# Kernel optimization log

Hardware: AMD Instinct MI355X
Metric: run time of the kernel (lower is better)

## Reference

```python
import math
import jax, jax.numpy as jnp
import numpy as np

B = 256          # graphs per batch
N0 = 512         # nodes per graph
DEG = 16         # avg degree
E = B * N0 * DEG # total edges
F_IN = 160
H = 64
RATIO = 0.11
NUM_CLASSES = 2


def setup_inputs() -> dict:
    key = jax.random.key(0)
    ks = jax.random.split(key, 20)
    x = jax.random.normal(ks[0], (B * N0, F_IN), jnp.float32)
    # within-graph random edges: src/dst local in [0, N0) plus graph offset
    eg = E // B
    off = (jnp.arange(B, dtype=jnp.int32) * N0)[:, None]
    src = (jax.random.randint(ks[1], (B, eg), 0, N0, jnp.int32) + off).reshape(-1)
    dst = (jax.random.randint(ks[2], (B, eg), 0, N0, jnp.int32) + off).reshape(-1)
    edge_index = jnp.stack([src, dst], 0)
    s = lambda fan: 1.0 / np.sqrt(fan)
    inp = {
        'x': x,
        'edge_index': edge_index,
        'conv1_Wr': jax.random.normal(ks[3], (F_IN, H), jnp.float32) * s(F_IN),
        'conv1_Wl': jax.random.normal(ks[4], (F_IN, H), jnp.float32) * s(F_IN),
        'conv1_b': jnp.zeros((H,), jnp.float32),
        'convs_Wr': jax.random.normal(ks[5], (5, H, H), jnp.float32) * s(H),
        'convs_Wl': jax.random.normal(ks[6], (5, H, H), jnp.float32) * s(H),
        'convs_b': jnp.zeros((5, H), jnp.float32),
        'pools_Wr': jax.random.normal(ks[7], (2, H, 1), jnp.float32) * s(H),
        'pools_Wl': jax.random.normal(ks[8], (2, H, 1), jnp.float32) * s(H),
        'pools_b': jnp.zeros((2, 1), jnp.float32),
        'lin1_W': jax.random.normal(ks[9], (6 * H, H), jnp.float32) * s(6 * H),
        'lin1_b': jnp.zeros((H,), jnp.float32),
        'lin2_W': jax.random.normal(ks[10], (H, NUM_CLASSES), jnp.float32) * s(H),
        'lin2_b': jnp.zeros((NUM_CLASSES,), jnp.float32),
    }
    return inp


def _gconv(x, src, dst, emask, Wr, Wl, b, n_nodes):
    # PyG GraphConv(aggr='mean'): lin_rel(mean_{j->i} x_j) + lin_root(x)
    msg = x[src] * emask[:, None]                              # [E, F]
    agg = jax.ops.segment_sum(msg, dst, num_segments=n_nodes)  # [N, F]
    deg = jax.ops.segment_sum(emask, dst, num_segments=n_nodes)
    agg = agg / jnp.maximum(deg, 1.0)[:, None]
    return agg @ Wr + b + x @ Wl


def _sag_pool(x, src, dst, emask, Wr, Wl, b, n_per, k):
    n_nodes = B * n_per
    score = _gconv(x, src, dst, emask, Wr, Wl, b, n_nodes)[:, 0]   # [N]
    _, idx = jax.lax.top_k(score.reshape(B, n_per), k)             # [B, k]
    perm = (idx + (jnp.arange(B, dtype=jnp.int32) * n_per)[:, None]).reshape(-1)
    new_x = x[perm] * jnp.tanh(score[perm])[:, None]
    newpos = jnp.full((n_nodes,), -1, jnp.int32).at[perm].set(
        jnp.arange(B * k, dtype=jnp.int32))
    ns, nd = newpos[src], newpos[dst]
    valid = (ns >= 0) & (nd >= 0)
    new_emask = emask * valid.astype(emask.dtype)
    return new_x, jnp.where(valid, ns, 0), jnp.where(valid, nd, 0), new_emask


def _gmp(x, n_per):  # global_mean_pool with equal-size graphs
    return x.reshape(B, n_per, -1).mean(axis=1)


def reference(x, edge_index, conv1_Wr, conv1_Wl, conv1_b, convs_Wr, convs_Wl,
              convs_b, pools_Wr, pools_Wl, pools_b, lin1_W, lin1_b,
              lin2_W, lin2_b):
    src, dst = edge_index[0], edge_index[1]
    emask = jnp.ones(src.shape, x.dtype)
    n = N0
    x = jax.nn.relu(_gconv(x, src, dst, emask, conv1_Wr, conv1_Wl, conv1_b, B * n))
    xs = [_gmp(x, n)]
    for i in range(5):
        x = jax.nn.relu(_gconv(x, src, dst, emask, convs_Wr[i], convs_Wl[i],
                               convs_b[i], B * n))
        xs.append(_gmp(x, n))
        if i % 2 == 0 and i < 4:
            j = i // 2
            k = math.ceil(RATIO * n)
            x, src, dst, emask = _sag_pool(x, src, dst, emask, pools_Wr[j],
                                           pools_Wl[j], pools_b[j], n, k)
            n = k
    h = jnp.concatenate(xs, axis=-1)          # JumpingKnowledge('cat') -> [B, 6H]
    h = jax.nn.relu(h @ lin1_W + lin1_b)
    h = h @ lin2_W + lin2_b                   # dropout is identity in eval mode
    return jax.nn.log_softmax(h, axis=-1)
```

## Files before the change

### kernel.cpp

```cpp
#include <hip/hip_runtime.h>
#include <math.h>

namespace {
constexpr int NB   = 256;
constexpr int EPG  = 8192;
constexpr int ETOT = NB * EPG;
}

__global__ __launch_bounds__(1024)
void mono(const float* __restrict__ x,
          const int* __restrict__ esrc, const int* __restrict__ edst,
          const float* __restrict__ c1Wr, const float* __restrict__ c1Wl,
          const float* __restrict__ c1b,
          const float* __restrict__ cWr, const float* __restrict__ cWl,
          const float* __restrict__ cb,
          const float* __restrict__ pwr, const float* __restrict__ pwl,
          const float* __restrict__ pb,
          const float* __restrict__ l1W, const float* __restrict__ l1b,
          const float* __restrict__ l2W, const float* __restrict__ l2b,
          float* __restrict__ out)
{
  __shared__ float zlds[512 * 64];
  __shared__ unsigned short csrbuf[EPG];
  __shared__ __align__(16) unsigned long long u2[512];
  __shared__ float wpf[2048];
  __shared__ float xsl[384];
  __shared__ int scnt;
  unsigned int* hist  = reinterpret_cast<unsigned int*>(u2);
  unsigned int* start = hist + 512;
  const int g = blockIdx.x, t = threadIdx.x;
  const int gbase = g * 512, ebase = g * EPG;
  const int lane = t & 63, w = t >> 6;
  const int ndbase = w * 32;

  auto stage_chunk = [&](int c, int p) {
    const int xb  = p ? 8192  : 0;
    const int wrO = p ? 18432 : 16384;
    const int wlO = p ? 22528 : 20480;
    #pragma unroll
    for (int i = 0; i < 2; ++i) {
      const int slot = t + i * 1024;
      const int r = slot >> 2, q = slot & 3;
      const float* gp = &x[(size_t)(gbase + r) * 160 + c * 16 + q * 4];
      float* lp = zlds + xb + (size_t)(i * 1024 + w * 64) * 4;
      __builtin_amdgcn_global_load_lds(
          (const __attribute__((address_space(1))) unsigned int*)gp,
          (__attribute__((address_space(3))) unsigned int*)lp, 16, 0, 0);
    }
    {
      const float* gp = &c1Wr[c * 1024 + t];
      float* lp = zlds + wrO + (size_t)(w * 64);
      __builtin_amdgcn_global_load_lds(
          (const __attribute__((address_space(1))) unsigned int*)gp,
          (__attribute__((address_space(3))) unsigned int*)lp, 4, 0, 0);
    }
    {
      const float* gp = &c1Wl[c * 1024 + t];
      float* lp = zlds + wlO + (size_t)(w * 64);
      __builtin_amdgcn_global_load_lds(
          (const __attribute__((address_space(1))) unsigned int*)gp,
          (__attribute__((address_space(3))) unsigned int*)lp, 4, 0, 0);
    }
  };

  if (t < 512) hist[t] = 0;
  if (t == 0) scnt = 0;
  __syncthreads();
  stage_chunk(0, 0);
  for (int e = t; e < EPG; e += 1024)
    atomicAdd(&hist[edst[ebase + e] - gbase], 1u);
  __syncthreads();
  {
    unsigned int* sA = reinterpret_cast<unsigned int*>(wpf);
    unsigned int* sB = sA + 512;
    if (t < 512) sA[t] = hist[t];
    __syncthreads();
    unsigned int *pa = sA, *pb = sB;
    for (int off = 1; off < 512; off <<= 1) {
      if (t < 512) {
        unsigned int v = pa[t];
        if (t >= off) v += pa[t - off];
        pb[t] = v;
      }
      __syncthreads();
      unsigned int* tmp = pa; pa = pb; pb = tmp;
    }
    if (t < 512) start[t] = pa[t] - hist[t];
    __syncthreads();
    unsigned int* cur = pb;
    if (t < 512) cur[t] = start[t];
    __syncthreads();
    for (int e = t; e < EPG; e += 1024) {
      const int sl = esrc[ebase + e] - gbase;
      const int dl = edst[ebase + e] - gbase;
      const unsigned int pos = atomicAdd(&cur[dl], 1u);
      csrbuf[pos] = (unsigned short)sl;
    }
  }
  __syncthreads();
  float zacc[32], xla[32];
  #pragma unroll
  for (int i = 0; i < 32; ++i) { zacc[i] = 0.f; xla[i] = 0.f; }
  #pragma unroll 1
  for (int c = 0; c < 10; ++c) {
    if (c < 9) stage_chunk(c + 1, (c + 1) & 1);
    const int p   = c & 1;
    const int xb  = p ? 8192  : 0;
    const int wrO = p ? 18432 : 16384;
    const int wlO = p ? 22528 : 20480;
    #pragma unroll 1
    for (int k4 = 0; k4 < 4; ++k4) {
      const int kb = k4 * 4;
      const float wr0 = zlds[wrO + (kb+0)*64 + lane], wr1 = zlds[wrO + (kb+1)*64 + lane],
                  wr2 = zlds[wrO + (kb+2)*64 + lane], wr3 = zlds[wrO + (kb+3)*64 + lane];
      const float wl0 = zlds[wlO + (kb+0)*64 + lane], wl1 = zlds[wlO + (kb+1)*64 + lane],
                  wl2 = zlds[wlO + (kb+2)*64 + lane], wl3 = zlds[wlO + (kb+3)*64 + lane];
      #pragma unroll
      for (int i = 0; i < 32; ++i) {
        const float4 xv = *reinterpret_cast<const float4*>(
            &zlds[xb + (ndbase + i) * 16 + kb]);
        float za = zacc[i], xa = xla[i];
        za = fmaf(xv.x, wr0, za); za = fmaf(xv.y, wr1, za);
        za = fmaf(xv.z, wr2, za); za = fmaf(xv.w, wr3, za);
        xa = fmaf(xv.x, wl0, xa); xa = fmaf(xv.y, wl1, xa);
        xa = fmaf(xv.z, wl2, xa); xa = fmaf(xv.w, wl3, xa);
        zacc[i] = za; xla[i] = xa;
      }
    }
    __syncthreads();
  }
  #pragma unroll
  for (int i = 0; i < 32; ++i)
    zlds[(ndbase + i) * 64 + lane] = zacc[i];
  __syncthreads();
  {
    const float bv = c1b[lane];
    float psum = 0.f;
    #pragma unroll 1
    for (int i = 0; i < 32; ++i) {
      const int nd = ndbase + i;
      const unsigned int s = start[nd], d = hist[nd];
      float a0 = 0.f, a1 = 0.f, a2 = 0.f, a3 = 0.f;
      unsigned int j = 0;
      for (; j + 4 <= d; j += 4) {
        const int i0 = csrbuf[s+j], i1 = csrbuf[s+j+1],
                  i2 = csrbuf[s+j+2], i3 = csrbuf[s+j+3];
        a0 += zlds[i0*64 + lane]; a1 += zlds[i1*64 + lane];
        a2 += zlds[i2*64 + lane]; a3 += zlds[i3*64 + lane];
      }
      for (; j < d; ++j) a0 += zlds[csrbuf[s+j]*64 + lane];
      float v = ((a0 + a1) + (a2 + a3)) / (float)(d > 0 ? d : 1) + xla[i] + bv;
      v = fmaxf(v, 0.f);
      zacc[i] = v;
      psum += v;
    }
    __syncthreads();
    #pragma unroll
    for (int i = 0; i < 32; ++i)
      zlds[(ndbase + i) * 64 + lane] = zacc[i];
    wpf[w * 64 + lane] = psum;
    __syncthreads();
    if (t < 64) {
      float s = 0.f;
      #pragma unroll
      for (int ww = 0; ww < 16; ++ww) s += wpf[ww*64 + t];
      xsl[0 + t] = s * (1.f/512.f);
    }
  }
  #pragma unroll
  for (int i = 0; i < 32; ++i) { zacc[i] = 0.f; xla[i] = 0.f; }
  {
    float* w_r = wpf;
    float* w_l = wpf + 1024;
    #pragma unroll 1
    for (int c = 0; c < 4; ++c) {
      __syncthreads();
      w_r[t] = cWr[c * 1024 + t];
      w_l[t] = cWl[c * 1024 + t];
      __syncthreads();
      #pragma unroll 1
      for (int k4 = 0; k4 < 4; ++k4) {
        const int kb = k4 * 4;
        const float wr0 = w_r[(kb+0)*64 + lane], wr1 = w_r[(kb+1)*64 + lane],
                    wr2 = w_r[(kb+2)*64 + lane], wr3 = w_r[(kb+3)*64 + lane];
        const float wl0 = w_l[(kb+0)*64 + lane], wl1 = w_l[(kb+1)*64 + lane],
                    wl2 = w_l[(kb+2)*64 + lane], wl3 = w_l[(kb+3)*64 + lane];
        #pragma unroll
        for (int i = 0; i < 32; ++i) {
          const float4 xv = *reinterpret_cast<const float4*>(
              &zlds[(ndbase + i) * 64 + c * 16 + kb]);
          float za = zacc[i], xa = xla[i];
          za = fmaf(xv.x, wr0, za); za = fmaf(xv.y, wr1, za);
          za = fmaf(xv.z, wr2, za); za = fmaf(xv.w, wr3, za);
          xa = fmaf(xv.x, wl0, xa); xa = fmaf(xv.y, wl1, xa);
          xa = fmaf(xv.z, wl2, xa); xa = fmaf(xv.w, wl3, xa);
          zacc[i] = za; xla[i] = xa;
        }
      }
    }
  }
  __syncthreads();
  #pragma unroll
  for (int i = 0; i < 32; ++i)
    zlds[(ndbase + i) * 64 + lane] = zacc[i];
  __syncthreads();
  {
    const float bv = cb[lane];
    float psum = 0.f;
    #pragma unroll 1
    for (int i = 0; i < 32; ++i) {
      const int nd = ndbase + i;
      const unsigned int s = start[nd], d = hist[nd];
      float a0 = 0.f, a1 = 0.f, a2 = 0.f, a3 = 0.f;
      unsigned int j = 0;
      for (; j + 4 <= d; j += 4) {
        const int i0 = csrbuf[s+j], i1 = csrbuf[s+j+1],
                  i2 = csrbuf[s+j+2], i3 = csrbuf[s+j+3];
        a0 += zlds[i0*64 + lane]; a1 += zlds[i1*64 + lane];
        a2 += zlds[i2*64 + lane]; a3 += zlds[i3*64 + lane];
      }
      for (; j < d; ++j) a0 += zlds[csrbuf[s+j]*64 + lane];
      float v = ((a0 + a1) + (a2 + a3)) / (float)(d > 0 ? d : 1) + xla[i] + bv;
      v = fmaxf(v, 0.f);
      zacc[i] = v;
      psum += v;
    }
    __syncthreads();
    #pragma unroll
    for (int i = 0; i < 32; ++i)
      zlds[(ndbase + i) * 64 + lane] = zacc[i];
    wpf[w * 64 + lane] = psum;
    __syncthreads();
    if (t < 64) {
      float s = 0.f;
      #pragma unroll
      for (int ww = 0; ww < 16; ++ww) s += wpf[ww*64 + t];
      xsl[64 + t] = s * (1.f/512.f);
    }
    __syncthreads();
  }
  {
    float* zs     = wpf;
    float* swl    = wpf + 512;
    float* sscore = wpf + 1024;
    const float pwrv = pwr[lane], pwlv = pwl[lane];
    for (int nd = w; nd < 512; nd += 16) {
      const float v = zlds[nd*64 + lane];
      float a = v * pwrv, b = v * pwlv;
      #pragma unroll
      for (int off = 32; off > 0; off >>= 1) {
        a += __shfl_xor(a, off);
        b += __shfl_xor(b, off);
      }
      if (lane == 0) { zs[nd] = a; swl[nd] = b; }
    }
    __syncthreads();
    if (t < 512) {
      const unsigned int s = start[t], d = hist[t];
      float a = 0.f;
      for (unsigned int j = 0; j < d; ++j) a += zs[csrbuf[s + j]];
      sscore[t] = a / fmaxf((float)d, 1.f) + pb[0] + swl[t];
    }
    __syncthreads();
    unsigned long long* keys = u2;
    if (t < 512) {
      unsigned int u = __float_as_uint(sscore[t]);
      u = (u & 0x80000000u) ? ~u : (u | 0x80000000u);
      keys[t] = ((unsigned long long)u << 32) | (unsigned int)(~(unsigned int)t);
    }
    __syncthreads();
    for (int kk = 2; kk <= 512; kk <<= 1) {
      for (int j = kk >> 1; j > 0; j >>= 1) {
        if (t < 512) {
          const int ixj = t ^ j;
          if (ixj > t) {
            const unsigned long long a = keys[t], bk = keys[ixj];
            const bool up = ((t & kk) == 0);
            if (up ? (a < bk) : (a > bk)) { keys[t] = bk; keys[ixj] = a; }
          }
        }
        __syncthreads();
      }
    }
    short* np = reinterpret_cast<short*>(csrbuf);
    if (t < 512) np[t] = -1;
    __syncthreads();
    if (t < 57)
      np[(int)(~(unsigned int)(keys[t] & 0xffffffffull))] = (short)t;
    __syncthreads();
    float xr[4];
    int nr = 0;
    for (int r = w * 4; r < w * 4 + 4 && r < 57; ++r) {
      const int old = (int)(~(unsigned int)(keys[r] & 0xffffffffull));
      xr[nr++] = zlds[old*64 + lane] * tanhf(sscore[old]);
    }
    if (t < 64) wpf[t] = 0.f;
    if (t == 0) scnt = 0;
    __syncthreads();
    nr = 0;
    for (int r = w * 4; r < w * 4 + 4 && r < 57; ++r)
      zlds[r*64 + lane] = xr[nr++];
    unsigned int* eb = reinterpret_cast<unsigned int*>(zlds + 16384);
    for (int e = t; e < EPG; e += 1024) {
      const int sl = esrc[ebase + e] - gbase;
      const int dl = edst[ebase + e] - gbase;
      const int ns = np[sl], nd2 = np[dl];
      if (ns >= 0 && nd2 >= 0) {
        const int slot = atomicAdd(&scnt, 1);
        eb[slot] = (unsigned int)ns | ((unsigned int)nd2 << 16);
        atomicAdd(&wpf[nd2], 1.f);
      }
    }
    __syncthreads();
  }
  const int m0 = scnt;
  float* X   = zlds;
  float* Z   = zlds + 4096;
  float* ACC = zlds + 8192;
  float* deg = wpf;
  float* w_s = wpf + 512;
  unsigned int* eb  = reinterpret_cast<unsigned int*>(zlds + 16384);
  unsigned int* eb1 = reinterpret_cast<unsigned int*>(zlds + 24576);

  auto conv57 = [&](int n, const unsigned int* edges, int m,
                    const float* Wr, const float* Wl, const float* bias,
                    int xs_off) {
    for (int i = t; i < n*64; i += 1024) { Z[i] = 0.f; ACC[i] = 0.f; }
    __syncthreads();
    for (int kc = 0; kc < 4; ++kc) {
      w_s[t] = Wr[kc*1024 + t];
      __syncthreads();
      for (int r = w; r < n; r += 16) {
        float za = 0.f;
        #pragma unroll
        for (int k = 0; k < 16; ++k)
          za = fmaf(X[r*64 + kc*16 + k], w_s[k*64 + lane], za);
        Z[r*64 + lane] += za;
      }
      __syncthreads();
    }
    for (int e = w; e < m; e += 16) {
      const unsigned int pr = edges[e];
      const int sl = pr & 0xffff, dl = pr >> 16;
      atomicAdd(&ACC[dl*64 + lane], Z[sl*64 + lane]);
    }
    __syncthreads();
    for (int i = t; i < n*64; i += 1024) {
      const int r = i >> 6, f = i & 63;
      Z[i] = ACC[i] / fmaxf(deg[r], 1.f) + bias[f];
    }
    __syncthreads();
    for (int kc = 0; kc < 4; ++kc) {
      w_s[t] = Wl[kc*1024 + t];
      __syncthreads();
      for (int r = w; r < n; r += 16) {
        float za = 0.f;
        #pragma unroll
        for (int k = 0; k < 16; ++k)
          za = fmaf(X[r*64 + kc*16 + k], w_s[k*64 + lane], za);
        Z[r*64 + lane] += za;
      }
      __syncthreads();
    }
    for (int i = t; i < n*64; i += 1024) X[i] = fmaxf(Z[i], 0.f);
    __syncthreads();
    float psum = 0.f;
    for (int r = w; r < n; r += 16) psum += X[r*64 + lane];
    Z[w*64 + lane] = psum;
    __syncthreads();
    if (t < 64) {
      float s = 0.f;
      #pragma unroll
      for (int ww = 0; ww < 16; ++ww) s += Z[ww*64 + t];
      xsl[xs_off + t] = s / (float)n;
    }
    __syncthreads();
  };

  conv57(57, eb, m0, cWr + 4096, cWl + 4096, cb + 64, 128);
  conv57(57, eb, m0, cWr + 8192, cWl + 8192, cb + 128, 192);

  {
    float* zs1 = wpf + 1536;
    float* sw1 = wpf + 1600;
    float* ss1 = wpf + 1664;
    const float pwrv = pwr[64 + lane], pwlv = pwl[64 + lane];
    for (int r = w; r < 57; r += 16) {
      float a = X[r*64 + lane] * pwrv, b = X[r*64 + lane] * pwlv;
      #pragma unroll
      for (int off = 32; off > 0; off >>= 1) {
        a += __shfl_xor(a, off);
        b += __shfl_xor(b, off);
      }
      if (lane == 0) { zs1[r] = a; sw1[r] = b; }
    }
    if (t >= 64 && t < 128) ACC[t - 64] = 0.f;
    __syncthreads();
    for (int e = t; e < m0; e += 1024) {
      const unsigned int pr = eb[e];
      atomicAdd(&ACC[pr >> 16], zs1[pr & 0xffff]);
    }
    __syncthreads();
    if (t < 57) ss1[t] = ACC[t] / fmaxf(deg[t], 1.f) + pb[1] + sw1[t];
    __syncthreads();
    unsigned long long* keys = u2;
    if (t < 64) {
      unsigned long long key = 0ull;
      if (t < 57) {
        unsigned int u = __float_as_uint(ss1[t]);
        u = (u & 0x80000000u) ? ~u : (u | 0x80000000u);
        key = ((unsigned long long)u << 32) | (unsigned int)(~(unsigned int)t);
      }
      keys[t] = key;
    }
    __syncthreads();
    for (int kk = 2; kk <= 64; kk <<= 1) {
      for (int j = kk >> 1; j > 0; j >>= 1) {
        if (t < 64) {
          const int ixj = t ^ j;
          if (ixj > t) {
            const unsigned long long a = keys[t], bk = keys[ixj];
            const bool up = ((t & kk) == 0);
            if (up ? (a < bk) : (a > bk)) { keys[t] = bk; keys[ixj] = a; }
          }
        }
        __syncthreads();
      }
    }
    short* np1 = reinterpret_cast<short*>(csrbuf);
    if (t < 64) np1[t] = -1;
    __syncthreads();
    if (t < 7)
      np1[(int)(~(unsigned int)(keys[t] & 0xffffffffull))] = (short)t;
    __syncthreads();
    float xv7 = 0.f;
    int old7 = -1;
    if (w < 7 && w * 4 == w * 4) {
      old7 = (int)(~(unsigned int)(keys[w] & 0xffffffffull));
      xv7 = X[old7*64 + lane] * tanhf(ss1[old7]);
    }
    if (t < 64) deg[t] = 0.f;
    if (t == 0) scnt = 0;
    __syncthreads();
    if (w < 7) X[w*64 + lane] = xv7;
    for (int e = t; e < m0; e += 1024) {
      const unsigned int pr = eb[e];
      const int ns = np1[pr & 0xffff], nd2 = np1[pr >> 16];
      if (ns >= 0 && nd2 >= 0) {
        const int slot = atomicAdd(&scnt, 1);
        eb1[slot] = (unsigned int)ns | ((unsigned int)nd2 << 16);
        atomicAdd(&deg[nd2], 1.f);
      }
    }
    __syncthreads();
  }
  const int m1 = scnt;

  conv57(7, eb1, m1, cWr + 12288, cWl + 12288, cb + 192, 256);
  conv57(7, eb1, m1, cWr + 16384, cWl + 16384, cb + 256, 320);

  if (t < 64) {
    float acc = l1b[t];
    for (int j = 0; j < 384; ++j) acc = fmaf(xsl[j], l1W[j*64 + t], acc);
    wpf[t] = fmaxf(acc, 0.f);
  }
  __syncthreads();
  if (t < 2) {
    float a2 = l2b[t];
    for (int f2 = 0; f2 < 64; ++f2) a2 = fmaf(wpf[f2], l2W[f2*2 + t], a2);
    wpf[64 + t] = a2;
  }
  __syncthreads();
  if (t < 2) {
    const float mx = fmaxf(wpf[64], wpf[65]);
    const float lse = mx + logf(expf(wpf[64]-mx) + expf(wpf[65]-mx));
    out[g*2 + t] = wpf[64 + t] - lse;
  }
}

extern "C" void kernel_launch(void* const* d_in, const int* in_sizes, int n_in,
                              void* d_out, int out_size, void* d_ws, size_t ws_size,
                              hipStream_t stream)
{
  (void)in_sizes; (void)n_in; (void)d_ws; (void)ws_size; (void)out_size;
  const float* x    = (const float*)d_in[0];
  const int*   ei   = (const int*)d_in[1];
  const float* c1Wr = (const float*)d_in[2];
  const float* c1Wl = (const float*)d_in[3];
  const float* c1b  = (const float*)d_in[4];
  const float* cWr  = (const float*)d_in[5];
  const float* cWl  = (const float*)d_in[6];
  const float* cb   = (const float*)d_in[7];
  const float* pWr  = (const float*)d_in[8];
  const float* pWl  = (const float*)d_in[9];
  const float* pb   = (const float*)d_in[10];
  const float* l1W  = (const float*)d_in[11];
  const float* l1b  = (const float*)d_in[12];
  const float* l2W  = (const float*)d_in[13];
  const float* l2b  = (const float*)d_in[14];
  float* out = (float*)d_out;
  const int* esrc = ei;
  const int* edst = ei + ETOT;

  mono<<<NB, 1024, 0, stream>>>(x, esrc, edst, c1Wr, c1Wl, c1b,
                                cWr, cWl, cb, pWr, pWl, pb,
                                l1W, l1b, l2W, l2b, out);
}
```

Before: 320.4 us.

## Use wavefront shuffles for scan and bitonic sorts, fuse conv57 matmuls

Replaces the LDS Hillis-Steele prefix scan with a wave-level shuffle scan plus a cross-wave offset, cutting the number of block barriers. The 512-key bitonic sort keeps keys in registers and uses shuffles for distances below 64, touching LDS only for larger strides. The 64-key sort runs entirely inside one wavefront. conv57 stages the full 64x64 weights in LDS once per matmul instead of in four chunks and fuses ReLU and the pooling sum into the second matmul, which removes several barriers and passes over the data.

```diff
diff --git a/kernel.cpp b/kernel.cpp
--- a/kernel.cpp
+++ b/kernel.cpp
@@ -28,6 +28,7 @@
   __shared__ int scnt;
   unsigned int* hist  = reinterpret_cast<unsigned int*>(u2);
   unsigned int* start = hist + 512;
+  unsigned int* curp  = reinterpret_cast<unsigned int*>(wpf);
   const int g = blockIdx.x, t = threadIdx.x;
   const int gbase = g * 512, ebase = g * EPG;
   const int lane = t & 63, w = t >> 6;
@@ -71,29 +72,31 @@
     atomicAdd(&hist[edst[ebase + e] - gbase], 1u);
   __syncthreads();
   {
-    unsigned int* sA = reinterpret_cast<unsigned int*>(wpf);
-    unsigned int* sB = sA + 512;
-    if (t < 512) sA[t] = hist[t];
-    __syncthreads();
-    unsigned int *pa = sA, *pb = sB;
-    for (int off = 1; off < 512; off <<= 1) {
-      if (t < 512) {
-        unsigned int v = pa[t];
-        if (t >= off) v += pa[t - off];
-        pb[t] = v;
-      }
-      __syncthreads();
-      unsigned int* tmp = pa; pa = pb; pb = tmp;
-    }
-    if (t < 512) start[t] = pa[t] - hist[t];
-    __syncthreads();
-    unsigned int* cur = pb;
-    if (t < 512) cur[t] = start[t];
+    unsigned int v = 0;
+    if (t < 512) {
+      v = hist[t];
+      #pragma unroll
+      for (int off = 1; off < 64; off <<= 1) {
+        const unsigned int up = __shfl_up(v, off);
+        if (lane >= off) v += up;
+      }
+      if (lane == 63)
+        reinterpret_cast<unsigned int*>(wpf)[1024 + w] = v;
+    }
+    __syncthreads();
+    if (t < 512) {
+      unsigned int off = 0;
+      for (int i = 0; i < w; ++i)
+        off += reinterpret_cast<unsigned int*>(wpf)[1024 + i];
+      const unsigned int st = off + v - hist[t];
+      start[t] = st;
+      curp[t]  = st;
+    }
     __syncthreads();
     for (int e = t; e < EPG; e += 1024) {
       const int sl = esrc[ebase + e] - gbase;
       const int dl = edst[ebase + e] - gbase;
-      const unsigned int pos = atomicAdd(&cur[dl], 1u);
+      const unsigned int pos = atomicAdd(&curp[dl], 1u);
       csrbuf[pos] = (unsigned short)sl;
     }
   }
@@ -262,26 +265,36 @@
       sscore[t] = a / fmaxf((float)d, 1.f) + pb[0] + swl[t];
     }
     __syncthreads();
-    unsigned long long* keys = u2;
+    unsigned long long k = 0ull;
     if (t < 512) {
       unsigned int u = __float_as_uint(sscore[t]);
       u = (u & 0x80000000u) ? ~u : (u | 0x80000000u);
-      keys[t] = ((unsigned long long)u << 32) | (unsigned int)(~(unsigned int)t);
-    }
-    __syncthreads();
+      k = ((unsigned long long)u << 32) | (unsigned int)(~(unsigned int)t);
+    }
     for (int kk = 2; kk <= 512; kk <<= 1) {
       for (int j = kk >> 1; j > 0; j >>= 1) {
-        if (t < 512) {
-          const int ixj = t ^ j;
-          if (ixj > t) {
-            const unsigned long long a = keys[t], bk = keys[ixj];
-            const bool up = ((t & kk) == 0);
-            if (up ? (a < bk) : (a > bk)) { keys[t] = bk; keys[ixj] = a; }
+        if (j >= 64) {
+          if (t < 512) u2[t] = k;
+          __syncthreads();
+          unsigned long long kp = 0ull;
+          if (t < 512) kp = u2[t ^ j];
+          __syncthreads();
+          if (t < 512) {
+            const bool keep_max = (((t & kk) == 0) == ((t & j) == 0));
+            k = keep_max ? (k >= kp ? k : kp) : (k >= kp ? kp : k);
           }
+        } else if (t < 512) {
+          const unsigned int lo = __shfl_xor((unsigned int)k, j);
+          const unsigned int hi = __shfl_xor((unsigned int)(k >> 32), j);
+          const unsigned long long kp = ((unsigned long long)hi << 32) | lo;
+          const bool keep_max = (((t & kk) == 0) == ((t & j) == 0));
+          k = keep_max ? (k >= kp ? k : kp) : (k >= kp ? kp : k);
         }
-        __syncthreads();
-      }
-    }
+      }
+    }
+    if (t < 512) u2[t] = k;
+    __syncthreads();
+    unsigned long long* keys = u2;
     short* np = reinterpret_cast<short*>(csrbuf);
     if (t < 512) np[t] = -1;
     __syncthreads();
@@ -318,60 +331,51 @@
   float* Z   = zlds + 4096;
   float* ACC = zlds + 8192;
   float* deg = wpf;
-  float* w_s = wpf + 512;
   unsigned int* eb  = reinterpret_cast<unsigned int*>(zlds + 16384);
   unsigned int* eb1 = reinterpret_cast<unsigned int*>(zlds + 24576);
 
   auto conv57 = [&](int n, const unsigned int* edges, int m,
                     const float* Wr, const float* Wl, const float* bias,
                     int xs_off) {
-    for (int i = t; i < n*64; i += 1024) { Z[i] = 0.f; ACC[i] = 0.f; }
-    __syncthreads();
-    for (int kc = 0; kc < 4; ++kc) {
-      w_s[t] = Wr[kc*1024 + t];
-      __syncthreads();
-      for (int r = w; r < n; r += 16) {
-        float za = 0.f;
-        #pragma unroll
-        for (int k = 0; k < 16; ++k)
-          za = fmaf(X[r*64 + kc*16 + k], w_s[k*64 + lane], za);
-        Z[r*64 + lane] += za;
-      }
-      __syncthreads();
-    }
+    float* Wfull = zlds + 12288;
+    for (int i = t; i < n*64; i += 1024) ACC[i] = 0.f;
+    #pragma unroll
+    for (int i = 0; i < 4; ++i) Wfull[t + i*1024] = Wr[t + i*1024];
+    __syncthreads();
+    for (int r = w; r < n; r += 16) {
+      float za = 0.f;
+      for (int k = 0; k < 64; ++k)
+        za = fmaf(X[r*64 + k], Wfull[k*64 + lane], za);
+      Z[r*64 + lane] = za;
+    }
+    __syncthreads();
     for (int e = w; e < m; e += 16) {
       const unsigned int pr = edges[e];
-      const int sl = pr & 0xffff, dl = pr >> 16;
-      atomicAdd(&ACC[dl*64 + lane], Z[sl*64 + lane]);
-    }
+      atomicAdd(&ACC[(pr >> 16)*64 + lane], Z[(pr & 0xffff)*64 + lane]);
+    }
+    #pragma unroll
+    for (int i = 0; i < 4; ++i) Wfull[t + i*1024] = Wl[t + i*1024];
     __syncthreads();
     for (int i = t; i < n*64; i += 1024) {
       const int r = i >> 6, f = i & 63;
       Z[i] = ACC[i] / fmaxf(deg[r], 1.f) + bias[f];
     }
     __syncthreads();
-    for (int kc = 0; kc < 4; ++kc) {
-      w_s[t] = Wl[kc*1024 + t];
-      __syncthreads();
-      for (int r = w; r < n; r += 16) {
-        float za = 0.f;
-        #pragma unroll
-        for (int k = 0; k < 16; ++k)
-          za = fmaf(X[r*64 + kc*16 + k], w_s[k*64 + lane], za);
-        Z[r*64 + lane] += za;
-      }
-      __syncthreads();
-    }
-    for (int i = t; i < n*64; i += 1024) X[i] = fmaxf(Z[i], 0.f);
-    __syncthreads();
     float psum = 0.f;
-    for (int r = w; r < n; r += 16) psum += X[r*64 + lane];
-    Z[w*64 + lane] = psum;
+    for (int r = w; r < n; r += 16) {
+      float za = Z[r*64 + lane];
+      for (int k = 0; k < 64; ++k)
+        za = fmaf(X[r*64 + k], Wfull[k*64 + lane], za);
+      za = fmaxf(za, 0.f);
+      X[r*64 + lane] = za;
+      psum += za;
+    }
+    ACC[w*64 + lane] = psum;
     __syncthreads();
     if (t < 64) {
       float s = 0.f;
       #pragma unroll
-      for (int ww = 0; ww < 16; ++ww) s += Z[ww*64 + t];
+      for (int ww = 0; ww < 16; ++ww) s += ACC[ww*64 + t];
       xsl[xs_off + t] = s / (float)n;
     }
     __syncthreads();
@@ -403,30 +407,26 @@
     __syncthreads();
     if (t < 57) ss1[t] = ACC[t] / fmaxf(deg[t], 1.f) + pb[1] + sw1[t];
     __syncthreads();
+    if (w == 0) {
+      unsigned long long k1 = 0ull;
+      if (lane < 57) {
+        unsigned int u = __float_as_uint(ss1[lane]);
+        u = (u & 0x80000000u) ? ~u : (u | 0x80000000u);
+        k1 = ((unsigned long long)u << 32) | (unsigned int)(~(unsigned int)lane);
+      }
+      for (int kk = 2; kk <= 64; kk <<= 1) {
+        for (int j = kk >> 1; j > 0; j >>= 1) {
+          const unsigned int lo = __shfl_xor((unsigned int)k1, j);
+          const unsigned int hi = __shfl_xor((unsigned int)(k1 >> 32), j);
+          const unsigned long long kp = ((unsigned long long)hi << 32) | lo;
+          const bool keep_max = (((lane & kk) == 0) == ((lane & j) == 0));
+          k1 = keep_max ? (k1 >= kp ? k1 : kp) : (k1 >= kp ? kp : k1);
+        }
+      }
+      u2[lane] = k1;
+    }
+    __syncthreads();
     unsigned long long* keys = u2;
-    if (t < 64) {
-      unsigned long long key = 0ull;
-      if (t < 57) {
-        unsigned int u = __float_as_uint(ss1[t]);
-        u = (u & 0x80000000u) ? ~u : (u | 0x80000000u);
-        key = ((unsigned long long)u << 32) | (unsigned int)(~(unsigned int)t);
-      }
-      keys[t] = key;
-    }
-    __syncthreads();
-    for (int kk = 2; kk <= 64; kk <<= 1) {
-      for (int j = kk >> 1; j > 0; j >>= 1) {
-        if (t < 64) {
-          const int ixj = t ^ j;
-          if (ixj > t) {
-            const unsigned long long a = keys[t], bk = keys[ixj];
-            const bool up = ((t & kk) == 0);
-            if (up ? (a < bk) : (a > bk)) { keys[t] = bk; keys[ixj] = a; }
-          }
-        }
-        __syncthreads();
-      }
-    }
     short* np1 = reinterpret_cast<short*>(csrbuf);
     if (t < 64) np1[t] = -1;
     __syncthreads();
@@ -434,9 +434,8 @@
       np1[(int)(~(unsigned int)(keys[t] & 0xffffffffull))] = (short)t;
     __syncthreads();
     float xv7 = 0.f;
-    int old7 = -1;
-    if (w < 7 && w * 4 == w * 4) {
-      old7 = (int)(~(unsigned int)(keys[w] & 0xffffffffull));
+    if (w < 7) {
+      const int old7 = (int)(~(unsigned int)(keys[w] & 0xffffffffull));
       xv7 = X[old7*64 + lane] * tanhf(ss1[old7]);
     }
     if (t < 64) deg[t] = 0.f;
```

New measurement: 317.1 us. Within noise of the previous version (-1.0%).
